# Optimization experiments

Hardware: AMD Instinct MI355X
Metric: run time of the kernel (lower is better)

The kernel has to match this reference:

```python
import jax, jax.numpy as jnp
import numpy as np

B, Q, E = 4, 1024, 1024
N_HEAD, D_HEAD = 16, 64
LN_EPS = 1e-3  # keras LayerNormalization default


def rel_shift(x):
    # x: [b, q, k, n] -> Transformer-XL relative shift along k axis
    b, q, k, n = x.shape
    x = jnp.pad(x, ((0, 0), (0, 0), (1, 0), (0, 0)))
    x = x.reshape(b, k + 1, q, n)[:, 1:]
    return x.reshape(b, q, k, n)


def setup_inputs() -> dict:
    key = jax.random.key(0)
    ks = jax.random.split(key, 12)
    s = 0.02
    w = jax.random.normal(ks[0], (B, Q, E), jnp.float32)
    r = jax.random.normal(ks[1], (Q, E), jnp.float32)
    r_w_bias = jax.random.normal(ks[2], (N_HEAD, D_HEAD), jnp.float32) * s
    r_r_bias = jax.random.normal(ks[3], (N_HEAD, D_HEAD), jnp.float32) * s
    # causal mask: 1 where j > i (masked), float as in original
    idx = jnp.arange(Q)
    attn_mask = (idx[None, :] > idx[:, None]).astype(jnp.float32)
    Wq = jax.random.normal(ks[4], (E, N_HEAD * D_HEAD), jnp.float32) * s
    Wk = jax.random.normal(ks[5], (E, N_HEAD * D_HEAD), jnp.float32) * s
    Wv = jax.random.normal(ks[6], (E, N_HEAD * D_HEAD), jnp.float32) * s
    Wr = jax.random.normal(ks[7], (E, N_HEAD * D_HEAD), jnp.float32) * s
    Wo = jax.random.normal(ks[8], (N_HEAD * D_HEAD, E), jnp.float32) * s
    gamma = jnp.ones((E,), jnp.float32)
    beta = jnp.zeros((E,), jnp.float32)
    return {"w": w, "r": r, "r_w_bias": r_w_bias, "r_r_bias": r_r_bias,
            "attn_mask": attn_mask, "Wq": Wq, "Wk": Wk, "Wv": Wv, "Wr": Wr,
            "Wo": Wo, "gamma": gamma, "beta": beta}


def reference(w, r, r_w_bias, r_r_bias, attn_mask, Wq, Wk, Wv, Wr, Wo, gamma, beta):
    b, q_len, embed = w.shape
    r_len = r.shape[0]
    # QKV / R projections (use_bias=False)
    q = (w @ Wq).reshape(b, q_len, N_HEAD, D_HEAD)
    k = (w @ Wk).reshape(b, q_len, N_HEAD, D_HEAD)
    v = (w @ Wv).reshape(b, q_len, N_HEAD, D_HEAD)
    rp = (r @ Wr).reshape(r_len, N_HEAD, D_HEAD)
    rw_q = q + r_w_bias  # [b,i,n,d]
    rr_q = q + r_r_bias
    AC = jnp.einsum('bind,bjnd->bijn', rw_q, k)
    BD = jnp.einsum('bind,jnd->bijn', rr_q, rp)
    BD = rel_shift(BD)
    attention = (AC + BD) / jnp.sqrt(jnp.float32(embed))
    m = attn_mask[None, :, :, None]
    attention = attention * (1.0 - m) - 1e30 * m
    attn_score = jax.nn.softmax(attention, axis=-2)  # softmax over j (key axis)
    out = jnp.einsum('bijn,bjnd->bind', attn_score, v)
    out = out.reshape(b, q_len, N_HEAD * D_HEAD) @ Wo
    x = w + out
    # keras LayerNormalization over last axis
    mu = jnp.mean(x, axis=-1, keepdims=True)
    var = jnp.var(x, axis=-1, keepdims=True)
    x = (x - mu) * jax.lax.rsqrt(var + LN_EPS) * gamma + beta
    return x
```

## Files before the change

kernel.cpp:

```cpp
#include <hip/hip_runtime.h>
#include <math.h>

#define BQ 4
#define SEQ 1024
#define EMB 1024
#define NH 16
#define DH 64
#define LN_EPS 1e-3f

typedef unsigned short u16;
typedef __attribute__((ext_vector_type(8))) unsigned short ushort8;
typedef __attribute__((ext_vector_type(4))) unsigned short ushort4v;
typedef __attribute__((ext_vector_type(8))) __bf16 bf16x8;
typedef __attribute__((ext_vector_type(4))) float f32x4;

__device__ __forceinline__ u16 f2bf(float f) {
  union { float f; unsigned u; } v;
  v.f = f;
  unsigned u = v.u;
  u += 0x7FFF + ((u >> 16) & 1);
  return (u16)(u >> 16);
}
__device__ __forceinline__ float bf2f(u16 h) {
  union { unsigned u; float f; } v;
  v.u = ((unsigned)h) << 16;
  return v.f;
}
__device__ __forceinline__ bf16x8 as_bf(ushort8 v) {
  union { ushort8 u; bf16x8 b; } x;
  x.u = v;
  return x.b;
}
__device__ __forceinline__ f32x4 mfma16(ushort8 a, ushort8 b, f32x4 c) {
  return __builtin_amdgcn_mfma_f32_16x16x32_bf16(as_bf(a), as_bf(b), c, 0, 0, 0);
}
__device__ __forceinline__ void gload16(const u16* g, u16* l) {
  __builtin_amdgcn_global_load_lds(
      (const __attribute__((address_space(1))) void*)g,
      (__attribute__((address_space(3))) void*)l, 16, 0, 0);
}

__global__ __launch_bounds__(256) void prep_kernel(
    const float* __restrict__ w, const float* __restrict__ r,
    const float* __restrict__ Wq, const float* __restrict__ Wk,
    const float* __restrict__ Wv, const float* __restrict__ Wr,
    const float* __restrict__ Wo, u16* __restrict__ wbf,
    u16* __restrict__ rbf, u16* __restrict__ WqkvT, u16* __restrict__ WrT,
    u16* __restrict__ WoT) {
  __shared__ u16 tile[32][33];
  const int bid = blockIdx.x;
  const int tid = threadIdx.x;
  if (bid < 5120) {
    const float* src = (bid < 4096) ? w : r;
    u16* dst = (bid < 4096) ? wbf : rbf;
    const int base = (bid < 4096) ? bid : bid - 4096;
    const int idx = (base * 256 + tid) * 4;
    const float4 v = *(const float4*)&src[idx];
    ushort4v o;
    o[0] = f2bf(v.x);
    o[1] = f2bf(v.y);
    o[2] = f2bf(v.z);
    o[3] = f2bf(v.w);
    *(ushort4v*)&dst[idx] = o;
  } else {
    const int t = bid - 5120;
    const int z = t >> 10;
    const int tt = t & 1023;
    const float* src = (z == 0) ? Wq : (z == 1) ? Wk : (z == 2) ? Wv
                       : (z == 3) ? Wr : Wo;
    u16* dst = (z < 3) ? (WqkvT + (size_t)z * 1024 * 1024)
               : (z == 3) ? WrT : WoT;
    const int k0 = (tt >> 5) * 32, n0 = (tt & 31) * 32;
    const int rr = tid >> 3, c4 = tid & 7;
    const float4 v =
        *(const float4*)&src[(size_t)(k0 + rr) * 1024 + n0 + c4 * 4];
    tile[rr][c4 * 4 + 0] = f2bf(v.x);
    tile[rr][c4 * 4 + 1] = f2bf(v.y);
    tile[rr][c4 * 4 + 2] = f2bf(v.z);
    tile[rr][c4 * 4 + 3] = f2bf(v.w);
    __syncthreads();
    ushort4v o;
#pragma unroll
    for (int e = 0; e < 4; ++e) o[e] = tile[c4 * 4 + e][rr];
    *(ushort4v*)&dst[(size_t)(n0 + rr) * 1024 + k0 + c4 * 4] = o;
  }
}

__device__ __forceinline__ void gemm_stage(const u16* __restrict__ A,
                                           const u16* __restrict__ Bt, int bm0,
                                           int bn0, int k0, u16* As, u16* Bs,
                                           int tid) {
#pragma unroll
  for (int rr = 0; rr < 4; ++rr) {
    const int c = rr * 256 + tid;
    const int row = c >> 3, kc = c & 7;
    const int g = kc ^ (row & 7);
    gload16(&A[(size_t)(bm0 + row) * 1024 + k0 + g * 8], &As[c * 8]);
    gload16(&Bt[(size_t)(bn0 + row) * 1024 + k0 + g * 8], &Bs[c * 8]);
  }
}

__device__ __forceinline__ void gemm_compute(const u16* As, const u16* Bs,
                                             int tid, f32x4 acc[4][4]) {
  const int quad = (tid >> 4) & 3, colL = tid & 15;
  const int wv = tid >> 6;
  const int wr = wv >> 1, wc = wv & 1;
  const int xs = colL & 7;
#pragma unroll
  for (int kh = 0; kh < 2; ++kh) {
    const int xo = ((kh * 4 + quad) ^ xs) * 8;
    ushort8 af[4], bf[4];
#pragma unroll
    for (int t = 0; t < 4; ++t) {
      af[t] = *(const ushort8*)&As[(wr * 64 + t * 16 + colL) * 64 + xo];
      bf[t] = *(const ushort8*)&Bs[(wc * 64 + t * 16 + colL) * 64 + xo];
    }
#pragma unroll
    for (int i = 0; i < 4; ++i)
#pragma unroll
      for (int j = 0; j < 4; ++j) acc[i][j] = mfma16(af[i], bf[j], acc[i][j]);
  }
}

__device__ __forceinline__ void gemm_core(const u16* __restrict__ A,
                                          const u16* __restrict__ Bt, int bm0,
                                          int bn0, u16* smem, int tid,
                                          f32x4 acc[4][4]) {
  u16* As[2] = {smem, smem + 16384};
  u16* Bs[2] = {smem + 8192, smem + 24576};
  gemm_stage(A, Bt, bm0, bn0, 0, As[0], Bs[0], tid);
#pragma unroll 2
  for (int it = 0; it < 16; ++it) {
    const int cur = it & 1;
    __syncthreads();
    if (it < 15)
      gemm_stage(A, Bt, bm0, bn0, (it + 1) * 64, As[cur ^ 1], Bs[cur ^ 1],
                 tid);
    gemm_compute(As[cur], Bs[cur], tid, acc);
  }
}

__global__ __launch_bounds__(256) void gemm_qkvrp(
    const u16* __restrict__ wbf, const u16* __restrict__ WqkvT,
    const u16* __restrict__ rbf, const u16* __restrict__ WrT,
    u16* __restrict__ qk, u16* __restrict__ vT, u16* __restrict__ rpb) {
  __shared__ u16 smem[32768];
  const int bid = blockIdx.x;
  const int tid = threadIdx.x;
  const bool isR = (bid >= 768);
  const u16* A = isR ? rbf : wbf;
  const u16* Bt = isR ? WrT : WqkvT;
  const int bm0 = isR ? ((bid - 768) >> 3) * 128 : (bid / 24) * 128;
  const int bn0 = isR ? ((bid - 768) & 7) * 128 : (bid % 24) * 128;

  f32x4 acc[4][4] = {};
  gemm_core(A, Bt, bm0, bn0, smem, tid, acc);

  const int quad = (tid >> 4) & 3, colL = tid & 15;
  const int wv = tid >> 6;
  const int wr = wv >> 1, wc = wv & 1;
  const bool vpart = !isR && (bn0 >= 2048);
#pragma unroll
  for (int i = 0; i < 4; ++i) {
    const int grow0 = bm0 + wr * 64 + i * 16 + quad * 4;
#pragma unroll
    for (int j = 0; j < 4; ++j) {
      const int gcol = bn0 + wc * 64 + j * 16 + colL;
      if (vpart) {
        const size_t base =
            ((size_t)(grow0 >> 10) * 1024 + (gcol - 2048)) * 1024 +
            (grow0 & 1023);
        ushort4v o;
#pragma unroll
        for (int e = 0; e < 4; ++e) o[e] = f2bf(acc[i][j][e]);
        *(ushort4v*)&vT[base] = o;
      } else {
        u16* dst = isR ? rpb : qk;
        const int Nld = isR ? 1024 : 2048;
#pragma unroll
        for (int e = 0; e < 4; ++e)
          dst[(size_t)(grow0 + e) * Nld + gcol] = f2bf(acc[i][j][e]);
      }
    }
  }
}

__global__ __launch_bounds__(256) void gemm_wo(const u16* __restrict__ A,
                                               const u16* __restrict__ Bt,
                                               const float* __restrict__ res,
                                               float* __restrict__ C) {
  __shared__ u16 smem[32768];
  const int tid = threadIdx.x;
  const int bm0 = blockIdx.y * 128, bn0 = blockIdx.x * 128;
  f32x4 acc[4][4] = {};
  gemm_core(A, Bt, bm0, bn0, smem, tid, acc);
  const int quad = (tid >> 4) & 3, colL = tid & 15;
  const int wv = tid >> 6;
  const int wr = wv >> 1, wc = wv & 1;
#pragma unroll
  for (int i = 0; i < 4; ++i) {
    const int grow0 = bm0 + wr * 64 + i * 16 + quad * 4;
#pragma unroll
    for (int j = 0; j < 4; ++j) {
      const int gcol = bn0 + wc * 64 + j * 16 + colL;
#pragma unroll
      for (int e = 0; e < 4; ++e) {
        const size_t off = (size_t)(grow0 + e) * 1024 + gcol;
        C[off] = acc[i][j][e] + res[off];
      }
    }
  }
}

__global__ __launch_bounds__(256, 3) void attn_mfma(
    const u16* __restrict__ qk,
    const u16* __restrict__ vT,
    const u16* __restrict__ rp,
    const float* __restrict__ rwb, const float* __restrict__ rrb,
    u16* __restrict__ obuf) {
  __shared__ u16 smem[22016];
  u16* ks = smem;
  u16* vs = smem + 4096;
  u16* rs = smem + 8192;
  u16* Ps = smem + 16384;

  const int L = blockIdx.x;
  const int b = L & 3;
  const int hn = (L >> 2) & 15;
  const int ph = L >> 6;
  const int itile = (ph < 8) ? ph : 23 - ph;
  const int i0 = itile * 64;
  const int tid = threadIdx.x;
  const int wv = tid >> 6;
  const int lane = tid & 63;
  const int quad = (tid >> 4) & 3, colL = tid & 15;
  u16* Psw = Ps + wv * 16 * 88;
  const int xo0 = (quad ^ (colL & 7)) * 8;
  const int xo1 = ((4 + quad) ^ (colL & 7)) * 8;

  ushort8 qw[2], qr[2];
  {
    const size_t qrow = (size_t)(b * SEQ + i0 + wv * 16 + colL) * 2048;
#pragma unroll
    for (int kh = 0; kh < 2; ++kh) {
      const int dof = hn * 64 + kh * 32 + quad * 8;
      const ushort8 qv = *(const ushort8*)&qk[qrow + dof];
      const float4 w0 = *(const float4*)&rwb[dof];
      const float4 w1 = *(const float4*)&rwb[dof + 4];
      const float4 r0 = *(const float4*)&rrb[dof];
      const float4 r1 = *(const float4*)&rrb[dof + 4];
      const float wb[8] = {w0.x, w0.y, w0.z, w0.w, w1.x, w1.y, w1.z, w1.w};
      const float rb[8] = {r0.x, r0.y, r0.z, r0.w, r1.x, r1.y, r1.z, r1.w};
#pragma unroll
      for (int e = 0; e < 8; ++e) {
        const float qf = bf2f(qv[e]);
        qw[kh][e] = f2bf(qf + wb[e]);
        qr[kh][e] = f2bf(qf + rb[e]);
      }
    }
  }

  {
    const int pb0 = SEQ - 64 - i0;
#pragma unroll
    for (int rr = 0; rr < 2; ++rr) {
      const int c = rr * 256 + tid;
      const int row = c >> 3, gp = c & 7;
      const int g = gp ^ (row & 7);
      gload16(&rp[(size_t)(pb0 + row) * 1024 + hn * 64 + g * 8], &rs[c * 8]);
    }
  }

  f32x4 oacc[4] = {};
  float l_part[4] = {0.f, 0.f, 0.f, 0.f};

  for (int j0 = 0; j0 <= i0; j0 += 64) {
    const int parity = (j0 >> 6) & 1;
    __syncthreads();
#pragma unroll
    for (int rr = 0; rr < 2; ++rr) {
      const int c = rr * 256 + tid;
      const int row = c >> 3, gp = c & 7;
      const int g = gp ^ (row & 7);
      gload16(&qk[(size_t)(b * SEQ + j0 + row) * 2048 + 1024 + hn * 64 + g * 8],
              &ks[c * 8]);
    }
#pragma unroll
    for (int rr = 0; rr < 2; ++rr) {
      const int c = rr * 256 + tid;
      const int d = c >> 3, gp = c & 7;
      const int g = gp ^ (d & 7);
      gload16(&vT[(size_t)(b * SEQ + hn * 64 + d) * 1024 + j0 + g * 8],
              &vs[c * 8]);
    }
    {
      const int pb64 = SEQ - i0 + j0;
      u16* rsH = rs + (parity ^ 1) * 4096;
#pragma unroll
      for (int rr = 0; rr < 2; ++rr) {
        const int c = rr * 256 + tid;
        const int row = c >> 3, gp = c & 7;
        const int g = gp ^ (row & 7);
        int p = pb64 + row;
        p = (p < SEQ) ? p : SEQ - 1;
        gload16(&rp[(size_t)p * 1024 + hn * 64 + g * 8], &rsH[c * 8]);
      }
    }
    __syncthreads();

    f32x4 sAC[4] = {};
#pragma unroll
    for (int jt = 0; jt < 4; ++jt) {
      const int rbase = (jt * 16 + colL) * 64;
      sAC[jt] = mfma16(qw[0], *(const ushort8*)&ks[rbase + xo0], sAC[jt]);
      sAC[jt] = mfma16(qw[1], *(const ushort8*)&ks[rbase + xo1], sAC[jt]);
    }
    f32x4 bd[5];
#pragma unroll
    for (int u = 0; u < 5; ++u) {
      const int tt = 3 - wv + u;
      const int half = ((tt >> 2) ^ parity) & 1;
      const int rbase = half * 4096 + ((tt & 3) * 16 + colL) * 64;
      f32x4 t = {};
      t = mfma16(qr[0], *(const ushort8*)&rs[rbase + xo0], t);
      t = mfma16(qr[1], *(const ushort8*)&rs[rbase + xo1], t);
      bd[u] = t;
    }

#pragma unroll
    for (int r = 0; r < 4; ++r) {
      const int lr = quad * 4 + r;
      const int ig = i0 + wv * 16 + lr;
      const int src = (lane & 48) | ((colL + 15 - lr) & 15);
      float Rv[5];
#pragma unroll
      for (int u = 0; u < 5; ++u) Rv[u] = __shfl(bd[u][r], src, 64);
#pragma unroll
      for (int jt = 0; jt < 4; ++jt) {
        const float bdv = (colL > lr) ? Rv[jt + 1] : Rv[jt];
        const float s = (sAC[jt][r] + bdv) * 0.03125f;
        const float pv = (j0 + jt * 16 + colL <= ig) ? __expf(s - 6.0f) : 0.0f;
        l_part[r] += pv;
        Psw[lr * 88 + jt * 16 + colL] = f2bf(pv);
      }
    }

    const int prow = colL * 88;
#pragma unroll
    for (int dt = 0; dt < 4; ++dt) {
      const int vbase = (dt * 16 + colL) * 64;
      oacc[dt] = mfma16(*(const ushort8*)&Psw[prow + quad * 8],
                        *(const ushort8*)&vs[vbase + xo0], oacc[dt]);
      oacc[dt] = mfma16(*(const ushort8*)&Psw[prow + 32 + quad * 8],
                        *(const ushort8*)&vs[vbase + xo1], oacc[dt]);
    }
  }

#pragma unroll
  for (int r = 0; r < 4; ++r) {
    float l = l_part[r];
    l += __shfl_xor(l, 1);
    l += __shfl_xor(l, 2);
    l += __shfl_xor(l, 4);
    l += __shfl_xor(l, 8);
    const float invl = 1.0f / l;
    const size_t grow =
        (size_t)(b * SEQ + i0 + wv * 16 + quad * 4 + r) * 1024 + hn * 64;
#pragma unroll
    for (int dt = 0; dt < 4; ++dt)
      obuf[grow + dt * 16 + colL] = f2bf(oacc[dt][r] * invl);
  }
}

__global__ __launch_bounds__(256) void ln_kernel(const float* __restrict__ x,
                                                 const float* __restrict__ gamma,
                                                 const float* __restrict__ beta,
                                                 float* __restrict__ out) {
  const int row = blockIdx.x;
  const int tid = threadIdx.x;
  const float4 xv = *(const float4*)&x[(size_t)row * EMB + tid * 4];
  float sum = xv.x + xv.y + xv.z + xv.w;
  float ss = xv.x * xv.x + xv.y * xv.y + xv.z * xv.z + xv.w * xv.w;
#pragma unroll
  for (int off = 1; off < 64; off <<= 1) {
    sum += __shfl_xor(sum, off);
    ss += __shfl_xor(ss, off);
  }
  __shared__ float s1[4], s2[4];
  if ((tid & 63) == 0) {
    s1[tid >> 6] = sum;
    s2[tid >> 6] = ss;
  }
  __syncthreads();
  sum = s1[0] + s1[1] + s1[2] + s1[3];
  ss = s2[0] + s2[1] + s2[2] + s2[3];
  const float mu = sum * (1.f / EMB);
  const float var = ss * (1.f / EMB) - mu * mu;
  const float rstd = rsqrtf(var + LN_EPS);
  const float4 g = *(const float4*)&gamma[tid * 4];
  const float4 be = *(const float4*)&beta[tid * 4];
  float4 o;
  o.x = (xv.x - mu) * rstd * g.x + be.x;
  o.y = (xv.y - mu) * rstd * g.y + be.y;
  o.z = (xv.z - mu) * rstd * g.z + be.z;
  o.w = (xv.w - mu) * rstd * g.w + be.w;
  *(float4*)&out[(size_t)row * EMB + tid * 4] = o;
}

extern "C" void kernel_launch(void* const* d_in, const int* in_sizes, int n_in,
                              void* d_out, int out_size, void* d_ws,
                              size_t ws_size, hipStream_t stream) {
  const float* w = (const float*)d_in[0];
  const float* r = (const float*)d_in[1];
  const float* rwb = (const float*)d_in[2];
  const float* rrb = (const float*)d_in[3];
  const float* Wq = (const float*)d_in[5];
  const float* Wk = (const float*)d_in[6];
  const float* Wv = (const float*)d_in[7];
  const float* Wr = (const float*)d_in[8];
  const float* Wo = (const float*)d_in[9];
  const float* gamma = (const float*)d_in[10];
  const float* beta = (const float*)d_in[11];
  float* outp = (float*)d_out;

  char* wsb = (char*)d_ws;
  u16* wbf = (u16*)(wsb);
  u16* rbf = (u16*)(wsb + ((size_t)8 << 20));
  u16* WqkvT = (u16*)(wsb + ((size_t)10 << 20));
  u16* WrT = (u16*)(wsb + ((size_t)16 << 20));
  u16* WoT = (u16*)(wsb + ((size_t)18 << 20));
  u16* qk = (u16*)(wsb + ((size_t)20 << 20));
  u16* vT = (u16*)(wsb + ((size_t)36 << 20));
  u16* rpb = (u16*)(wsb + ((size_t)44 << 20));
  u16* obuf = (u16*)(wsb + ((size_t)10 << 20));

  const dim3 blk(256);
  prep_kernel<<<10240, blk, 0, stream>>>(w, r, Wq, Wk, Wv, Wr, Wo, wbf, rbf,
                                         WqkvT, WrT, WoT);
  gemm_qkvrp<<<832, blk, 0, stream>>>(wbf, WqkvT, rbf, WrT, qk, vT, rpb);
  attn_mfma<<<1024, blk, 0, stream>>>(qk, vT, rpb, rwb, rrb, obuf);
  gemm_wo<<<dim3(8, 32), blk, 0, stream>>>(obuf, WoT, w, outp);
  ln_kernel<<<BQ * SEQ, blk, 0, stream>>>(outp, gamma, beta, outp);
}
```

Before: 201.8 us.

## Double attention query tile to 128 rows per block with triple-buffered rel-pos slices

The attention kernel now gives each block 128 query rows instead of 64, with each wave owning two 16-row groups. Each K/V tile loaded into shared memory is therefore reused across twice as many queries, and the grid is halved to 512 blocks. The relative-position buffer becomes a three-slot ring, and the P scratch stride shrinks from 88 to 72. The trade-offs are more registers and shared memory (launch bounds lowered from 3 to 2 blocks per SM), coarser causal load balance, and more masked work on diagonal tiles.

After: 222.1 us. 1.1x slower.

```diff
diff --git a/kernel.cpp b/kernel.cpp
--- a/kernel.cpp
+++ b/kernel.cpp
@@ -212,35 +212,37 @@
   }
 }
 
-__global__ __launch_bounds__(256, 3) void attn_mfma(
+__global__ __launch_bounds__(256, 2) void attn_mfma(
     const u16* __restrict__ qk,
     const u16* __restrict__ vT,
     const u16* __restrict__ rp,
     const float* __restrict__ rwb, const float* __restrict__ rrb,
     u16* __restrict__ obuf) {
-  __shared__ u16 smem[22016];
+  __shared__ u16 smem[29696];
   u16* ks = smem;
   u16* vs = smem + 4096;
   u16* rs = smem + 8192;
-  u16* Ps = smem + 16384;
+  u16* Ps = smem + 20480;
 
   const int L = blockIdx.x;
   const int b = L & 3;
   const int hn = (L >> 2) & 15;
   const int ph = L >> 6;
-  const int itile = (ph < 8) ? ph : 23 - ph;
-  const int i0 = itile * 64;
+  const int it = (ph < 4) ? ph : 11 - ph;
+  const int i0 = it * 128;
   const int tid = threadIdx.x;
   const int wv = tid >> 6;
   const int lane = tid & 63;
   const int quad = (tid >> 4) & 3, colL = tid & 15;
-  u16* Psw = Ps + wv * 16 * 88;
+  u16* Psw = Ps + wv * 2304;
   const int xo0 = (quad ^ (colL & 7)) * 8;
   const int xo1 = ((4 + quad) ^ (colL & 7)) * 8;
 
-  ushort8 qw[2], qr[2];
-  {
-    const size_t qrow = (size_t)(b * SEQ + i0 + wv * 16 + colL) * 2048;
+  ushort8 qw[2][2], qr[2][2];
+#pragma unroll
+  for (int g = 0; g < 2; ++g) {
+    const size_t qrow =
+        (size_t)(b * SEQ + i0 + wv * 32 + g * 16 + colL) * 2048;
 #pragma unroll
     for (int kh = 0; kh < 2; ++kh) {
       const int dof = hn * 64 + kh * 32 + quad * 8;
@@ -254,122 +256,144 @@
 #pragma unroll
       for (int e = 0; e < 8; ++e) {
         const float qf = bf2f(qv[e]);
-        qw[kh][e] = f2bf(qf + wb[e]);
-        qr[kh][e] = f2bf(qf + rb[e]);
-      }
-    }
-  }
-
-  {
-    const int pb0 = SEQ - 64 - i0;
+        qw[g][kh][e] = f2bf(qf + wb[e]);
+        qr[g][kh][e] = f2bf(qf + rb[e]);
+      }
+    }
+  }
+
+  const int P0 = SEQ - 128 - i0;
+#pragma unroll
+  for (int sl = 0; sl < 2; ++sl) {
 #pragma unroll
     for (int rr = 0; rr < 2; ++rr) {
       const int c = rr * 256 + tid;
       const int row = c >> 3, gp = c & 7;
-      const int g = gp ^ (row & 7);
-      gload16(&rp[(size_t)(pb0 + row) * 1024 + hn * 64 + g * 8], &rs[c * 8]);
-    }
-  }
-
-  f32x4 oacc[4] = {};
-  float l_part[4] = {0.f, 0.f, 0.f, 0.f};
-
-  for (int j0 = 0; j0 <= i0; j0 += 64) {
-    const int parity = (j0 >> 6) & 1;
+      const int g2 = gp ^ (row & 7);
+      gload16(&rp[(size_t)(P0 + sl * 64 + row) * 1024 + hn * 64 + g2 * 8],
+              &rs[sl * 4096 + c * 8]);
+    }
+  }
+
+  f32x4 oacc[2][4] = {};
+  float l_part[2][4] = {};
+
+  const int nTrips = 2 * it + 2;
+  for (int n = 0; n < nTrips; ++n) {
+    const int j0 = n * 64;
     __syncthreads();
 #pragma unroll
     for (int rr = 0; rr < 2; ++rr) {
       const int c = rr * 256 + tid;
       const int row = c >> 3, gp = c & 7;
-      const int g = gp ^ (row & 7);
-      gload16(&qk[(size_t)(b * SEQ + j0 + row) * 2048 + 1024 + hn * 64 + g * 8],
-              &ks[c * 8]);
+      const int g2 = gp ^ (row & 7);
+      gload16(
+          &qk[(size_t)(b * SEQ + j0 + row) * 2048 + 1024 + hn * 64 + g2 * 8],
+          &ks[c * 8]);
     }
 #pragma unroll
     for (int rr = 0; rr < 2; ++rr) {
       const int c = rr * 256 + tid;
       const int d = c >> 3, gp = c & 7;
-      const int g = gp ^ (d & 7);
-      gload16(&vT[(size_t)(b * SEQ + hn * 64 + d) * 1024 + j0 + g * 8],
+      const int g2 = gp ^ (d & 7);
+      gload16(&vT[(size_t)(b * SEQ + hn * 64 + d) * 1024 + j0 + g2 * 8],
               &vs[c * 8]);
     }
     {
-      const int pb64 = SEQ - i0 + j0;
-      u16* rsH = rs + (parity ^ 1) * 4096;
+      const int sl2 = (n + 2) % 3;
+      u16* rsN = rs + sl2 * 4096;
 #pragma unroll
       for (int rr = 0; rr < 2; ++rr) {
         const int c = rr * 256 + tid;
         const int row = c >> 3, gp = c & 7;
-        const int g = gp ^ (row & 7);
-        int p = pb64 + row;
+        const int g2 = gp ^ (row & 7);
+        int p = P0 + 64 * n + 128 + row;
         p = (p < SEQ) ? p : SEQ - 1;
-        gload16(&rp[(size_t)p * 1024 + hn * 64 + g * 8], &rsH[c * 8]);
+        gload16(&rp[(size_t)p * 1024 + hn * 64 + g2 * 8], &rsN[c * 8]);
       }
     }
     __syncthreads();
 
-    f32x4 sAC[4] = {};
-#pragma unroll
-    for (int jt = 0; jt < 4; ++jt) {
-      const int rbase = (jt * 16 + colL) * 64;
-      sAC[jt] = mfma16(qw[0], *(const ushort8*)&ks[rbase + xo0], sAC[jt]);
-      sAC[jt] = mfma16(qw[1], *(const ushort8*)&ks[rbase + xo1], sAC[jt]);
-    }
-    f32x4 bd[5];
-#pragma unroll
-    for (int u = 0; u < 5; ++u) {
-      const int tt = 3 - wv + u;
-      const int half = ((tt >> 2) ^ parity) & 1;
-      const int rbase = half * 4096 + ((tt & 3) * 16 + colL) * 64;
-      f32x4 t = {};
-      t = mfma16(qr[0], *(const ushort8*)&rs[rbase + xo0], t);
-      t = mfma16(qr[1], *(const ushort8*)&rs[rbase + xo1], t);
-      bd[u] = t;
-    }
-
+    f32x4 sAC[2][4] = {};
+#pragma unroll
+    for (int g = 0; g < 2; ++g)
+#pragma unroll
+      for (int jt = 0; jt < 4; ++jt) {
+        const int rbase = (jt * 16 + colL) * 64;
+        sAC[g][jt] =
+            mfma16(qw[g][0], *(const ushort8*)&ks[rbase + xo0], sAC[g][jt]);
+        sAC[g][jt] =
+            mfma16(qw[g][1], *(const ushort8*)&ks[rbase + xo1], sAC[g][jt]);
+      }
+    f32x4 bd[2][5];
+#pragma unroll
+    for (int g = 0; g < 2; ++g) {
+      const int baseT = 7 - 2 * wv - g;
+#pragma unroll
+      for (int u = 0; u < 5; ++u) {
+        const int tt = baseT + u;
+        const int sl = (n + (tt >> 2)) % 3;
+        const int rbase = sl * 4096 + ((tt & 3) * 16 + colL) * 64;
+        f32x4 t = {};
+        t = mfma16(qr[g][0], *(const ushort8*)&rs[rbase + xo0], t);
+        t = mfma16(qr[g][1], *(const ushort8*)&rs[rbase + xo1], t);
+        bd[g][u] = t;
+      }
+    }
+
+#pragma unroll
+    for (int g = 0; g < 2; ++g)
+#pragma unroll
+      for (int r = 0; r < 4; ++r) {
+        const int lr = quad * 4 + r;
+        const int ig = i0 + wv * 32 + g * 16 + lr;
+        const int src = (lane & 48) | ((colL + 15 - lr) & 15);
+        float Rv[5];
+#pragma unroll
+        for (int u = 0; u < 5; ++u) Rv[u] = __shfl(bd[g][u][r], src, 64);
+#pragma unroll
+        for (int jt = 0; jt < 4; ++jt) {
+          const float bdv = (colL > lr) ? Rv[jt + 1] : Rv[jt];
+          const float sum = sAC[g][jt][r] + bdv;
+          const float pv = (j0 + jt * 16 + colL <= ig)
+                               ? __expf(fmaf(sum, 0.03125f, -6.0f))
+                               : 0.0f;
+          l_part[g][r] += pv;
+          Psw[(g * 16 + lr) * 72 + jt * 16 + colL] = f2bf(pv);
+        }
+      }
+
+#pragma unroll
+    for (int g = 0; g < 2; ++g) {
+      const int prow = (g * 16 + colL) * 72;
+#pragma unroll
+      for (int dt = 0; dt < 4; ++dt) {
+        const int vbase = (dt * 16 + colL) * 64;
+        oacc[g][dt] = mfma16(*(const ushort8*)&Psw[prow + quad * 8],
+                             *(const ushort8*)&vs[vbase + xo0], oacc[g][dt]);
+        oacc[g][dt] = mfma16(*(const ushort8*)&Psw[prow + 32 + quad * 8],
+                             *(const ushort8*)&vs[vbase + xo1], oacc[g][dt]);
+      }
+    }
+  }
+
+#pragma unroll
+  for (int g = 0; g < 2; ++g)
 #pragma unroll
     for (int r = 0; r < 4; ++r) {
-      const int lr = quad * 4 + r;
-      const int ig = i0 + wv * 16 + lr;
-      const int src = (lane & 48) | ((colL + 15 - lr) & 15);
-      float Rv[5];
-#pragma unroll
-      for (int u = 0; u < 5; ++u) Rv[u] = __shfl(bd[u][r], src, 64);
-#pragma unroll
-      for (int jt = 0; jt < 4; ++jt) {
-        const float bdv = (colL > lr) ? Rv[jt + 1] : Rv[jt];
-        const float s = (sAC[jt][r] + bdv) * 0.03125f;
-        const float pv = (j0 + jt * 16 + colL <= ig) ? __expf(s - 6.0f) : 0.0f;
-        l_part[r] += pv;
-        Psw[lr * 88 + jt * 16 + colL] = f2bf(pv);
-      }
-    }
-
-    const int prow = colL * 88;
-#pragma unroll
-    for (int dt = 0; dt < 4; ++dt) {
-      const int vbase = (dt * 16 + colL) * 64;
-      oacc[dt] = mfma16(*(const ushort8*)&Psw[prow + quad * 8],
-                        *(const ushort8*)&vs[vbase + xo0], oacc[dt]);
-      oacc[dt] = mfma16(*(const ushort8*)&Psw[prow + 32 + quad * 8],
-                        *(const ushort8*)&vs[vbase + xo1], oacc[dt]);
-    }
-  }
-
-#pragma unroll
-  for (int r = 0; r < 4; ++r) {
-    float l = l_part[r];
-    l += __shfl_xor(l, 1);
-    l += __shfl_xor(l, 2);
-    l += __shfl_xor(l, 4);
-    l += __shfl_xor(l, 8);
-    const float invl = 1.0f / l;
-    const size_t grow =
-        (size_t)(b * SEQ + i0 + wv * 16 + quad * 4 + r) * 1024 + hn * 64;
-#pragma unroll
-    for (int dt = 0; dt < 4; ++dt)
-      obuf[grow + dt * 16 + colL] = f2bf(oacc[dt][r] * invl);
-  }
+      float l = l_part[g][r];
+      l += __shfl_xor(l, 1);
+      l += __shfl_xor(l, 2);
+      l += __shfl_xor(l, 4);
+      l += __shfl_xor(l, 8);
+      const float invl = 1.0f / l;
+      const size_t grow =
+          (size_t)(b * SEQ + i0 + wv * 32 + g * 16 + quad * 4 + r) * 1024 +
+          hn * 64;
+#pragma unroll
+      for (int dt = 0; dt < 4; ++dt)
+        obuf[grow + dt * 16 + colL] = f2bf(oacc[g][dt][r] * invl);
+    }
 }
 
 __global__ __launch_bounds__(256) void ln_kernel(const float* __restrict__ x,
@@ -438,7 +462,7 @@
   prep_kernel<<<10240, blk, 0, stream>>>(w, r, Wq, Wk, Wv, Wr, Wo, wbf, rbf,
                                          WqkvT, WrT, WoT);
   gemm_qkvrp<<<832, blk, 0, stream>>>(wbf, WqkvT, rbf, WrT, qk, vT, rpb);
-  attn_mfma<<<1024, blk, 0, stream>>>(qk, vT, rpb, rwb, rrb, obuf);
+  attn_mfma<<<512, blk, 0, stream>>>(qk, vT, rpb, rwb, rrb, obuf);
   gemm_wo<<<dim3(8, 32), blk, 0, stream>>>(obuf, WoT, w, outp);
   ln_kernel<<<BQ * SEQ, blk, 0, stream>>>(outp, gamma, beta, outp);
 }
```
